# Performance work log

Hardware: AMD Instinct MI355X
Metric: run time of the kernel (lower is better)

Reference implementation:

```python
import jax, jax.numpy as jnp
import numpy as np

B, T, I, H, O = 64, 512, 256, 512, 1


def _rnn_layer(x, W_ih, W_hh, b_ih, b_hh):
    """One ReLU-RNN layer. x: [B,T,D] -> [B,T,H]."""
    # Precompute input projection for all timesteps as one big GEMM.
    xw = jnp.einsum('btd,hd->bth', x, W_ih) + b_ih + b_hh  # [B,T,H]

    def step(h, xt):
        h = jax.nn.relu(xt + h @ W_hh.T)  # [B,H]
        return h, h

    h0 = jnp.zeros((x.shape[0], W_hh.shape[0]), x.dtype)
    _, out = jax.lax.scan(step, h0, jnp.swapaxes(xw, 0, 1))  # [T,B,H]
    return jnp.swapaxes(out, 0, 1)


def setup_inputs() -> dict:
    key = jax.random.key(0)
    ks = jax.random.split(key, 11)
    s_i = 1.0 / np.sqrt(H)
    inp = {
        'x': jax.random.normal(ks[0], (B, T, I), dtype=jnp.float32),
        'W_ih0': jax.random.uniform(ks[1], (H, I), jnp.float32, -s_i, s_i),
        'W_hh0': jax.random.uniform(ks[2], (H, H), jnp.float32, -s_i, s_i),
        'b_ih0': jax.random.uniform(ks[3], (H,), jnp.float32, -s_i, s_i),
        'b_hh0': jax.random.uniform(ks[4], (H,), jnp.float32, -s_i, s_i),
        'W_ih1': jax.random.uniform(ks[5], (H, H), jnp.float32, -s_i, s_i),
        'W_hh1': jax.random.uniform(ks[6], (H, H), jnp.float32, -s_i, s_i),
        'b_ih1': jax.random.uniform(ks[7], (H,), jnp.float32, -s_i, s_i),
        'b_hh1': jax.random.uniform(ks[8], (H,), jnp.float32, -s_i, s_i),
        'W_fc': jax.random.uniform(ks[9], (O, H), jnp.float32, -s_i, s_i),
        'b_fc': jax.random.uniform(ks[10], (O,), jnp.float32, -s_i, s_i),
    }
    return inp


def reference(x, W_ih0, W_hh0, b_ih0, b_hh0, W_ih1, W_hh1, b_ih1, b_hh1, W_fc, b_fc):
    h = _rnn_layer(x, W_ih0, W_hh0, b_ih0, b_hh0)   # layer 0
    h = _rnn_layer(h, W_ih1, W_hh1, b_ih1, b_hh1)   # layer 1
    logits = jnp.einsum('bth,oh->bto', h, W_fc) + b_fc
    return jax.nn.sigmoid(logits)  # [B,T,O]
```

## Files before the change

kernel.cpp:

```cpp
#include <hip/hip_runtime.h>


typedef _Float16 half8 __attribute__((ext_vector_type(8)));
typedef _Float16 half4 __attribute__((ext_vector_type(4)));
typedef float    f32x4 __attribute__((ext_vector_type(4)));

#define T_DIM 512
#define H_DIM 512
#define CHUNK 16

#define RAW_BARRIER() asm volatile("s_waitcnt lgkmcnt(0)\n\ts_barrier" ::: "memory")

__global__ __launch_bounds__(256) void conv_w_f16(
    const float* __restrict__ in, _Float16* __restrict__ out)
{
    int i = (blockIdx.x * 256 + threadIdx.x) * 4;
    float4 v = *(const float4*)(in + i);
    out[i + 0] = (_Float16)v.x;
    out[i + 1] = (_Float16)v.y;
    out[i + 2] = (_Float16)v.z;
    out[i + 3] = (_Float16)v.w;
}

__global__ __launch_bounds__(64) void init_flags(int* flags)
{
    flags[threadIdx.x] = 0;
}

#define WSTASH 0
#define HBUF   65536

__global__ __launch_bounds__(256, 1) void pipeline(
    const float* __restrict__ x,
    const float* __restrict__ Wih0,
    const float* __restrict__ bih0,
    const float* __restrict__ bhh0,
    const float* __restrict__ Wih1,
    const float* __restrict__ bih1,
    const float* __restrict__ bhh1,
    const _Float16* __restrict__ W16_0,
    const _Float16* __restrict__ W16_1,
    const float* __restrict__ wfc,
    _Float16* __restrict__ xwF0,
    _Float16* __restrict__ xwF1,
    _Float16* __restrict__ h0,
    float* __restrict__ part,
    int* __restrict__ flags)
{
    __shared__ _Float16 smem[73856];

    const int bx   = blockIdx.x;
    const int tid  = threadIdx.x;
    const int w    = tid >> 6;
    const int lane = tid & 63;
    const int col  = lane & 15;
    const int q    = lane >> 4;

    int* flag_xw0 = flags;
    int* flag_h0  = flags + 16;
    int* flag_xw1 = flags + 20;

    if (bx < 16) {
        const int g = bx >> 2, s = bx & 3;

        half8 wb[8][8];
        float bias[8];
#pragma unroll
        for (int nt = 0; nt < 8; ++nt) {
            int n = w * 128 + nt * 16 + col;
            bias[nt] = bih0[n] + bhh0[n];
#pragma unroll
            for (int kt = 0; kt < 8; ++kt) {
                const float* p = Wih0 + (size_t)n * 256 + kt * 32 + q * 8;
                float4 f0 = *(const float4*)p;
                float4 f1 = *(const float4*)(p + 4);
                half8 hv;
                hv[0]=(_Float16)f0.x; hv[1]=(_Float16)f0.y;
                hv[2]=(_Float16)f0.z; hv[3]=(_Float16)f0.w;
                hv[4]=(_Float16)f1.x; hv[5]=(_Float16)f1.y;
                hv[6]=(_Float16)f1.z; hv[7]=(_Float16)f1.w;
                wb[kt][nt] = hv;
            }
        }

        for (int c = 0; c < T_DIM / CHUNK; ++c) {
#pragma unroll
            for (int i = 0; i < 4; ++i) {
                int t = c * CHUNK + s * 4 + i;
                f32x4 acc[8] = {};
#pragma unroll
                for (int kt = 0; kt < 8; ++kt) {
                    const float* p = x + ((size_t)(g * 16 + col) * T_DIM + t) * 256
                                       + kt * 32 + q * 8;
                    float4 a0 = *(const float4*)p;
                    float4 a1 = *(const float4*)(p + 4);
                    half8 ah;
                    ah[0]=(_Float16)a0.x; ah[1]=(_Float16)a0.y;
                    ah[2]=(_Float16)a0.z; ah[3]=(_Float16)a0.w;
                    ah[4]=(_Float16)a1.x; ah[5]=(_Float16)a1.y;
                    ah[6]=(_Float16)a1.z; ah[7]=(_Float16)a1.w;
#pragma unroll
                    for (int nt = 0; nt < 8; ++nt)
                        acc[nt] = __builtin_amdgcn_mfma_f32_16x16x32_f16(
                            ah, wb[kt][nt], acc[nt], 0, 0, 0);
                }
                _Float16* dst = xwF0 + ((size_t)t * 4 + g) * 8192 + lane * 4;
#pragma unroll
                for (int nt = 0; nt < 8; ++nt) {
                    half4 hv;
#pragma unroll
                    for (int r = 0; r < 4; ++r)
                        hv[r] = (_Float16)(acc[nt][r] + bias[nt]);
                    *(half4*)(dst + (w * 8 + nt) * 256) = hv;
                }
            }
            __syncthreads();
            if (tid == 0)
                __hip_atomic_store(&flag_xw0[g * 4 + s], c + 1, __ATOMIC_RELEASE,
                                   __HIP_MEMORY_SCOPE_AGENT);
        }
        return;
    }

    if (bx < 32) {
        const int g = (bx - 16) >> 2, s = (bx - 16) & 3;

        half8 wb[12][8];
        float bias[8];
#pragma unroll
        for (int nt = 0; nt < 8; ++nt) {
            int n = w * 128 + nt * 16 + col;
            bias[nt] = bih1[n] + bhh1[n];
#pragma unroll
            for (int kt = 0; kt < 16; ++kt) {
                const float* p = Wih1 + (size_t)n * 512 + kt * 32 + q * 8;
                float4 f0 = *(const float4*)p;
                float4 f1 = *(const float4*)(p + 4);
                half8 hv;
                hv[0]=(_Float16)f0.x; hv[1]=(_Float16)f0.y;
                hv[2]=(_Float16)f0.z; hv[3]=(_Float16)f0.w;
                hv[4]=(_Float16)f1.x; hv[5]=(_Float16)f1.y;
                hv[6]=(_Float16)f1.z; hv[7]=(_Float16)f1.w;
                if (kt < 12) wb[kt][nt] = hv;
                else *(half8*)&smem[WSTASH + w * 16384
                                    + (((kt - 12) * 8 + nt) * 64 + lane) * 8] = hv;
            }
        }
        __syncthreads();

        for (int c = 0; c < T_DIM / CHUNK; ++c) {
            while (__hip_atomic_load(&flag_h0[g], __ATOMIC_ACQUIRE,
                                     __HIP_MEMORY_SCOPE_AGENT) < c + 1)
                __builtin_amdgcn_s_sleep(2);
#pragma unroll
            for (int i = 0; i < 4; ++i) {
                int t = c * CHUNK + s * 4 + i;
                f32x4 acc[8] = {};
#pragma unroll
                for (int kt = 0; kt < 16; ++kt) {
                    half8 ah = *(const half8*)(
                        h0 + ((size_t)(g * T_DIM + t) * 16 + col) * 512
                           + kt * 32 + q * 8);
#pragma unroll
                    for (int nt = 0; nt < 8; ++nt) {
                        half8 b;
                        if (kt < 12) b = wb[kt][nt];
                        else b = *(const half8*)&smem[WSTASH + w * 16384
                                 + (((kt - 12) * 8 + nt) * 64 + lane) * 8];
                        acc[nt] = __builtin_amdgcn_mfma_f32_16x16x32_f16(
                            ah, b, acc[nt], 0, 0, 0);
                    }
                }
                _Float16* dst = xwF1 + ((size_t)t * 4 + g) * 8192 + lane * 4;
#pragma unroll
                for (int nt = 0; nt < 8; ++nt) {
                    half4 hv;
#pragma unroll
                    for (int r = 0; r < 4; ++r)
                        hv[r] = (_Float16)(acc[nt][r] + bias[nt]);
                    *(half4*)(dst + (w * 8 + nt) * 256) = hv;
                }
            }
            __syncthreads();
            if (tid == 0)
                __hip_atomic_store(&flag_xw1[g * 4 + s], c + 1, __ATOMIC_RELEASE,
                                   __HIP_MEMORY_SCOPE_AGENT);
        }
        return;
    }

    const bool L0 = (bx < 36);
    const int  g  = L0 ? bx - 32 : bx - 36;
    const _Float16* W16 = L0 ? W16_0 : W16_1;
    const _Float16* xwF = L0 ? xwF0 : xwF1;
    int* waitf = L0 ? flag_xw0 : flag_xw1;

    for (int i = tid; i < 16 * 520; i += 256) smem[HBUF + i] = (_Float16)0.f;

#pragma unroll
    for (int kt4 = 0; kt4 < 4; ++kt4)
#pragma unroll
        for (int nt = 0; nt < 8; ++nt)
            *(half8*)&smem[WSTASH + w * 16384 + ((kt4 * 8 + nt) * 64 + lane) * 8] =
                *(const half8*)(W16 + (size_t)(w * 128 + nt * 16 + col) * 512
                                + (12 + kt4) * 32 + q * 8);
    half8 wreg[12][8];
#pragma unroll
    for (int kt = 0; kt < 12; ++kt)
#pragma unroll
        for (int nt = 0; nt < 8; ++nt)
            wreg[kt][nt] = *(const half8*)(
                W16 + (size_t)(w * 128 + nt * 16 + col) * 512 + kt * 32 + q * 8);

    float wfn[8] = {};
    if (!L0) {
#pragma unroll
        for (int nt = 0; nt < 8; ++nt) wfn[nt] = wfc[w * 128 + nt * 16 + col];
    }

    __syncthreads();

    for (int t = 0; t < T_DIM; ++t) {
        if ((t & (CHUNK - 1)) == 0) {
            int need = (t >> 4) + 1;
#pragma unroll
            for (int s4 = 0; s4 < 4; ++s4)
                while (__hip_atomic_load(&waitf[g * 4 + s4], __ATOMIC_ACQUIRE,
                                         __HIP_MEMORY_SCOPE_AGENT) < need)
                    __builtin_amdgcn_s_sleep(2);
        }

        half4 xv[8];
        {
            const _Float16* xwp = xwF + ((size_t)t * 4 + g) * 8192 + lane * 4;
#pragma unroll
            for (int nt = 0; nt < 8; ++nt)
                xv[nt] = *(const half4*)(xwp + (w * 8 + nt) * 256);
        }

        f32x4 acc[8] = {};
#pragma unroll
        for (int kt = 0; kt < 16; ++kt) {
            half8 a = *(const half8*)&smem[HBUF + col * 520 + kt * 32 + q * 8];
#pragma unroll
            for (int nt = 0; nt < 8; ++nt) {
                half8 b;
                if (kt < 12) b = wreg[kt][nt];
                else b = *(const half8*)&smem[WSTASH + w * 16384
                         + (((kt - 12) * 8 + nt) * 64 + lane) * 8];
                acc[nt] = __builtin_amdgcn_mfma_f32_16x16x32_f16(a, b, acc[nt], 0, 0, 0);
            }
        }
        RAW_BARRIER();

        float p0 = 0.f, p1 = 0.f, p2 = 0.f, p3 = 0.f;
#pragma unroll
        for (int nt = 0; nt < 8; ++nt) {
            int n = w * 128 + nt * 16 + col;
#pragma unroll
            for (int r = 0; r < 4; ++r) {
                float v = fmaxf(acc[nt][r] + (float)xv[nt][r], 0.f);
                smem[HBUF + (q * 4 + r) * 520 + n] = (_Float16)v;
                if (!L0) {
                    float pv = v * wfn[nt];
                    if (r == 0) p0 += pv; else if (r == 1) p1 += pv;
                    else if (r == 2) p2 += pv; else p3 += pv;
                }
            }
        }
        RAW_BARRIER();

        if (L0) {
            int m = w * 4 + q;
#pragma unroll
            for (int seg = 0; seg < 4; ++seg) {
                half8 hv = *(const half8*)&smem[HBUF + m * 520 + col * 32 + seg * 8];
                *(half8*)(h0 + ((size_t)(g * T_DIM + t) * 16 + m) * 512
                          + col * 32 + seg * 8) = hv;
            }
            if ((t & (CHUNK - 1)) == CHUNK - 1) {
                __syncthreads();
                if (tid == 0)
                    __hip_atomic_store(&flag_h0[g], (t >> 4) + 1, __ATOMIC_RELEASE,
                                       __HIP_MEMORY_SCOPE_AGENT);
            }
        } else {
#pragma unroll
            for (int s2 = 1; s2 < 16; s2 <<= 1) {
                p0 += __shfl_xor(p0, s2); p1 += __shfl_xor(p1, s2);
                p2 += __shfl_xor(p2, s2); p3 += __shfl_xor(p3, s2);
            }
            if (col == 0) {
                f32x4 pv = {p0, p1, p2, p3};
                *(f32x4*)(part + ((size_t)(g * 4 + w) * T_DIM + t) * 16 + q * 4) = pv;
            }
        }
    }
}

__global__ __launch_bounds__(256) void fc_epilogue(
    const float* __restrict__ part, const float* __restrict__ bfc,
    float* __restrict__ outp)
{
    int i = blockIdx.x * 256 + threadIdx.x;
    int b = i >> 9, t = i & 511;
    int g = b >> 4, m = b & 15;
    float s = bfc[0];
#pragma unroll
    for (int w = 0; w < 4; ++w)
        s += part[((size_t)(g * 4 + w) * T_DIM + t) * 16 + m];
    outp[i] = 1.f / (1.f + __expf(-s));
}

extern "C" void kernel_launch(void* const* d_in, const int* in_sizes, int n_in,
                              void* d_out, int out_size, void* d_ws, size_t ws_size,
                              hipStream_t stream)
{
    const float* x     = (const float*)d_in[0];
    const float* W_ih0 = (const float*)d_in[1];
    const float* W_hh0 = (const float*)d_in[2];
    const float* b_ih0 = (const float*)d_in[3];
    const float* b_hh0 = (const float*)d_in[4];
    const float* W_ih1 = (const float*)d_in[5];
    const float* W_hh1 = (const float*)d_in[6];
    const float* b_ih1 = (const float*)d_in[7];
    const float* b_hh1 = (const float*)d_in[8];
    const float* W_fc  = (const float*)d_in[9];
    const float* b_fc  = (const float*)d_in[10];

    _Float16* xwF0  = (_Float16*)d_ws;
    _Float16* xwF1  = xwF0 + (size_t)T_DIM * 4 * 8192;
    _Float16* h0    = xwF1 + (size_t)T_DIM * 4 * 8192;
    _Float16* W16_0 = h0 + (size_t)4 * T_DIM * 16 * 512;
    _Float16* W16_1 = W16_0 + (size_t)H_DIM * H_DIM;
    float*    partf = (float*)(W16_1 + (size_t)H_DIM * H_DIM);
    int*      flags = (int*)(partf + (size_t)16 * T_DIM * 16);

    init_flags<<<1, 64, 0, stream>>>(flags);
    conv_w_f16<<<256, 256, 0, stream>>>(W_hh0, W16_0);
    conv_w_f16<<<256, 256, 0, stream>>>(W_hh1, W16_1);

    pipeline<<<40, 256, 0, stream>>>(x, W_ih0, b_ih0, b_hh0,
                                     W_ih1, b_ih1, b_hh1,
                                     W16_0, W16_1, W_fc,
                                     xwF0, xwF1, h0, partf, flags);

    fc_epilogue<<<(64 * T_DIM) / 256, 256, 0, stream>>>(partf, b_fc, (float*)d_out);
}
```

Before: 1.724 ms.

## Double-buffer hidden state to drop a barrier and prefetch next-step inputs

The recurrent hidden state in shared memory becomes double-buffered, so each step reads one buffer and writes the other, and the barrier between the MFMA loop and the ReLU write-back goes away. The next timestep's input projection is now prefetched into registers before the barrier, and the flag wait is hoisted to one step ahead using relaxed loads followed by a single acquire fence. To make room for the second buffer, one weight column tile per k-slice moves from the LDS stash into registers, which raises register pressure. The aim is to cut per-step synchronisation and global-load latency on the serial recurrence critical path.

```diff
diff --git a/kernel.cpp b/kernel.cpp
--- a/kernel.cpp
+++ b/kernel.cpp
@@ -28,7 +28,8 @@
 }
 
 #define WSTASH 0
-#define HBUF   65536
+#define HBUF   57344
+#define HBUFSZ 8320
 
 __global__ __launch_bounds__(256, 1) void pipeline(
     const float* __restrict__ x,
@@ -47,7 +48,7 @@
     float* __restrict__ part,
     int* __restrict__ flags)
 {
-    __shared__ _Float16 smem[73856];
+    __shared__ _Float16 smem[73984];
 
     const int bx   = blockIdx.x;
     const int tid  = threadIdx.x;
@@ -193,17 +194,22 @@
     const int  g  = L0 ? bx - 32 : bx - 36;
     const _Float16* W16 = L0 ? W16_0 : W16_1;
     const _Float16* xwF = L0 ? xwF0 : xwF1;
-    int* waitf = L0 ? flag_xw0 : flag_xw1;
-
-    for (int i = tid; i < 16 * 520; i += 256) smem[HBUF + i] = (_Float16)0.f;
+    int* waitf = (L0 ? flag_xw0 : flag_xw1) + g * 4;
+
+    for (int i = tid; i < 2 * HBUFSZ; i += 256) smem[HBUF + i] = (_Float16)0.f;
 
 #pragma unroll
     for (int kt4 = 0; kt4 < 4; ++kt4)
 #pragma unroll
-        for (int nt = 0; nt < 8; ++nt)
-            *(half8*)&smem[WSTASH + w * 16384 + ((kt4 * 8 + nt) * 64 + lane) * 8] =
+        for (int nt = 0; nt < 7; ++nt)
+            *(half8*)&smem[WSTASH + w * 14336 + ((kt4 * 7 + nt) * 64 + lane) * 8] =
                 *(const half8*)(W16 + (size_t)(w * 128 + nt * 16 + col) * 512
                                 + (12 + kt4) * 32 + q * 8);
+    half8 wreg2[4];
+#pragma unroll
+    for (int kt4 = 0; kt4 < 4; ++kt4)
+        wreg2[kt4] = *(const half8*)(W16 + (size_t)(w * 128 + 7 * 16 + col) * 512
+                                     + (12 + kt4) * 32 + q * 8);
     half8 wreg[12][8];
 #pragma unroll
     for (int kt = 0; kt < 12; ++kt)
@@ -220,38 +226,45 @@
 
     __syncthreads();
 
+    auto wait4 = [&](int need) {
+        for (;;) {
+            int a0 = __hip_atomic_load(waitf + 0, __ATOMIC_RELAXED, __HIP_MEMORY_SCOPE_AGENT);
+            int a1 = __hip_atomic_load(waitf + 1, __ATOMIC_RELAXED, __HIP_MEMORY_SCOPE_AGENT);
+            int a2 = __hip_atomic_load(waitf + 2, __ATOMIC_RELAXED, __HIP_MEMORY_SCOPE_AGENT);
+            int a3 = __hip_atomic_load(waitf + 3, __ATOMIC_RELAXED, __HIP_MEMORY_SCOPE_AGENT);
+            if (a0 >= need && a1 >= need && a2 >= need && a3 >= need) break;
+            __builtin_amdgcn_s_sleep(2);
+        }
+        __builtin_amdgcn_fence(__ATOMIC_ACQUIRE, "agent");
+    };
+
+    wait4(1);
+    half4 xv[8];
+    {
+        const _Float16* xwp = xwF + (size_t)g * 8192 + lane * 4;
+#pragma unroll
+        for (int nt = 0; nt < 8; ++nt)
+            xv[nt] = *(const half4*)(xwp + (w * 8 + nt) * 256);
+    }
+
     for (int t = 0; t < T_DIM; ++t) {
-        if ((t & (CHUNK - 1)) == 0) {
-            int need = (t >> 4) + 1;
-#pragma unroll
-            for (int s4 = 0; s4 < 4; ++s4)
-                while (__hip_atomic_load(&waitf[g * 4 + s4], __ATOMIC_ACQUIRE,
-                                         __HIP_MEMORY_SCOPE_AGENT) < need)
-                    __builtin_amdgcn_s_sleep(2);
-        }
-
-        half4 xv[8];
-        {
-            const _Float16* xwp = xwF + ((size_t)t * 4 + g) * 8192 + lane * 4;
-#pragma unroll
-            for (int nt = 0; nt < 8; ++nt)
-                xv[nt] = *(const half4*)(xwp + (w * 8 + nt) * 256);
-        }
+        const int HR = HBUF + (t & 1) * HBUFSZ;
+        const int HW = HBUF + ((t & 1) ^ 1) * HBUFSZ;
 
         f32x4 acc[8] = {};
 #pragma unroll
         for (int kt = 0; kt < 16; ++kt) {
-            half8 a = *(const half8*)&smem[HBUF + col * 520 + kt * 32 + q * 8];
+            half8 a = *(const half8*)&smem[HR + col * 520 + kt * 32 + q * 8];
 #pragma unroll
             for (int nt = 0; nt < 8; ++nt) {
                 half8 b;
-                if (kt < 12) b = wreg[kt][nt];
-                else b = *(const half8*)&smem[WSTASH + w * 16384
-                         + (((kt - 12) * 8 + nt) * 64 + lane) * 8];
+                if (kt < 12)     b = wreg[kt][nt];
+                else if (nt < 7) b = *(const half8*)&smem[WSTASH + w * 14336
+                                     + (((kt - 12) * 7 + nt) * 64 + lane) * 8];
+                else             b = wreg2[kt - 12];
                 acc[nt] = __builtin_amdgcn_mfma_f32_16x16x32_f16(a, b, acc[nt], 0, 0, 0);
             }
         }
-        RAW_BARRIER();
 
         float p0 = 0.f, p1 = 0.f, p2 = 0.f, p3 = 0.f;
 #pragma unroll
@@ -260,7 +273,7 @@
 #pragma unroll
             for (int r = 0; r < 4; ++r) {
                 float v = fmaxf(acc[nt][r] + (float)xv[nt][r], 0.f);
-                smem[HBUF + (q * 4 + r) * 520 + n] = (_Float16)v;
+                smem[HW + (q * 4 + r) * 520 + n] = (_Float16)v;
                 if (!L0) {
                     float pv = v * wfn[nt];
                     if (r == 0) p0 += pv; else if (r == 1) p1 += pv;
@@ -268,13 +281,36 @@
                 }
             }
         }
+        if (!L0) {
+#pragma unroll
+            for (int s2 = 1; s2 < 16; s2 <<= 1) {
+                p0 += __shfl_xor(p0, s2); p1 += __shfl_xor(p1, s2);
+                p2 += __shfl_xor(p2, s2); p3 += __shfl_xor(p3, s2);
+            }
+            if (col == 0) {
+                f32x4 pv = {p0, p1, p2, p3};
+                *(f32x4*)(part + ((size_t)(g * 4 + w) * T_DIM + t) * 16 + q * 4) = pv;
+            }
+        }
+
+        const bool rel = L0 && ((t & (CHUNK - 1)) == CHUNK - 1);
+        if (t + 1 < T_DIM) {
+            if (((t + 1) & (CHUNK - 1)) == 0) wait4(((t + 1) >> 4) + 1);
+            if (!rel) {
+                const _Float16* xwp = xwF + ((size_t)(t + 1) * 4 + g) * 8192 + lane * 4;
+#pragma unroll
+                for (int nt = 0; nt < 8; ++nt)
+                    xv[nt] = *(const half4*)(xwp + (w * 8 + nt) * 256);
+            }
+        }
+
         RAW_BARRIER();
 
         if (L0) {
             int m = w * 4 + q;
 #pragma unroll
             for (int seg = 0; seg < 4; ++seg) {
-                half8 hv = *(const half8*)&smem[HBUF + m * 520 + col * 32 + seg * 8];
+                half8 hv = *(const half8*)&smem[HW + m * 520 + col * 32 + seg * 8];
                 *(half8*)(h0 + ((size_t)(g * T_DIM + t) * 16 + m) * 512
                           + col * 32 + seg * 8) = hv;
             }
@@ -283,16 +319,12 @@
                 if (tid == 0)
                     __hip_atomic_store(&flag_h0[g], (t >> 4) + 1, __ATOMIC_RELEASE,
                                        __HIP_MEMORY_SCOPE_AGENT);
-            }
-        } else {
-#pragma unroll
-            for (int s2 = 1; s2 < 16; s2 <<= 1) {
-                p0 += __shfl_xor(p0, s2); p1 += __shfl_xor(p1, s2);
-                p2 += __shfl_xor(p2, s2); p3 += __shfl_xor(p3, s2);
-            }
-            if (col == 0) {
-                f32x4 pv = {p0, p1, p2, p3};
-                *(f32x4*)(part + ((size_t)(g * 4 + w) * T_DIM + t) * 16 + q * 4) = pv;
+                if (t + 1 < T_DIM) {
+                    const _Float16* xwp = xwF + ((size_t)(t + 1) * 4 + g) * 8192 + lane * 4;
+#pragma unroll
+                    for (int nt = 0; nt < 8; ++nt)
+                        xv[nt] = *(const half4*)(xwp + (w * 8 + nt) * 256);
+                }
             }
         }
     }
```

Result: slower. 1.812 ms (+5.1%).
